# Kernel optimization log

Measured on AMD Instinct MI355X. Metric: run time of the kernel, lower is better.

The kernel has to match this reference:

```python
import jax, jax.numpy as jnp
import numpy as np

N = 50000
E = 800000
IN_C, HID, OUT_C = 512, 256, 128


def gcn_conv(x, edge_index, W, b, num_nodes):
    # PyG GCNConv: add self-loops, symmetric normalization, linear-then-aggregate.
    h = x @ W  # [N, out]
    src = jnp.concatenate([edge_index[0], jnp.arange(num_nodes)])
    dst = jnp.concatenate([edge_index[1], jnp.arange(num_nodes)])
    ones = jnp.ones(src.shape[0], dtype=x.dtype)
    deg = jax.ops.segment_sum(ones, dst, num_segments=num_nodes)  # in-degree incl. self-loop
    dinv = jax.lax.rsqrt(deg)  # deg >= 1 thanks to self-loops
    norm = dinv[src] * dinv[dst]  # [E+N]
    msg = h[src] * norm[:, None]  # gather + scale
    out = jax.ops.segment_sum(msg, dst, num_segments=num_nodes)  # scatter-add
    return out + b


def setup_inputs() -> dict:
    key = jax.random.key(0)
    k_x, k_e, k_w1, k_b1, k_w2, k_b2 = jax.random.split(key, 6)
    x = jax.random.normal(k_x, (N, IN_C), dtype=jnp.float32)
    edge_index = jax.random.randint(k_e, (2, E), 0, N, dtype=jnp.int64)
    s1 = 1.0 / np.sqrt(IN_C)
    s2 = 1.0 / np.sqrt(HID)
    W1 = jax.random.uniform(k_w1, (IN_C, HID), jnp.float32, -s1, s1)
    b1 = jax.random.uniform(k_b1, (HID,), jnp.float32, -s1, s1)
    W2 = jax.random.uniform(k_w2, (HID, OUT_C), jnp.float32, -s2, s2)
    b2 = jax.random.uniform(k_b2, (OUT_C,), jnp.float32, -s2, s2)
    return {"x": x, "edge_index": edge_index, "W1": W1, "b1": b1, "W2": W2, "b2": b2}


def reference(x, edge_index, W1, b1, W2, b2):
    h = gcn_conv(x, edge_index, W1, b1, N)
    h = jax.nn.relu(h)
    # dropout in eval mode == identity
    return gcn_conv(h, edge_index, W2, b2, N)
```

## Files before the change

kernel.cpp:

```cpp
#include <hip/hip_runtime.h>
#include <stdint.h>

typedef __bf16 bf16_t;
typedef bf16_t bf16x8 __attribute__((ext_vector_type(8)));
typedef bf16_t bf16x4 __attribute__((ext_vector_type(4)));
typedef bf16_t bf16x2 __attribute__((ext_vector_type(2)));
typedef float  f32x4  __attribute__((ext_vector_type(4)));

typedef __attribute__((address_space(3))) void* as3p;
typedef const __attribute__((address_space(1))) void* as1p;

#define IN_C 512
#define HID  256
#define OUTC 128

__global__ void k_prep(const float* __restrict__ W1, const float* __restrict__ W2,
                       const void* __restrict__ ei, int* __restrict__ flag,
                       int* __restrict__ cnt, bf16_t* __restrict__ W1t,
                       bf16_t* __restrict__ W2t, int n) {
  int t = blockIdx.x * blockDim.x + threadIdx.x;
  if (t < IN_C * HID) {
    W1t[(size_t)(t & 255) * IN_C + (t >> 8)] = (bf16_t)W1[t];
    return;
  }
  int u = t - IN_C * HID;
  if (u < HID * OUTC) {
    W2t[(size_t)(u & 127) * HID + (u >> 7)] = (bf16_t)W2[u];
    return;
  }
  u -= HID * OUTC;
  if (u < n) {
    cnt[u] = 0;
    return;
  }
  if (u == n) {
    const long long* p = (const long long*)ei;
    int ok = 1;
    for (int i = 0; i < 64; ++i) {
      long long v = p[i];
      if (v < 0 || v >= n) ok = 0;
    }
    *flag = ok;
  }
}

__global__ void k_hist(const void* __restrict__ ei, const int* __restrict__ flag,
                       int* __restrict__ cnt, int E) {
  int e = blockIdx.x * blockDim.x + threadIdx.x;
  if (e >= E) return;
  int d;
  if (*flag) d = (int)((const long long*)ei)[(size_t)E + e];
  else       d = ((const int*)ei)[E + e];
  atomicAdd(&cnt[d], 1);
}

__global__ void k_scan1(const int* __restrict__ cnt, int* __restrict__ ex,
                        int* __restrict__ part, float* __restrict__ dinv, int n) {
  __shared__ int sh[256];
  int i = blockIdx.x * 256 + threadIdx.x;
  int v = (i < n) ? cnt[i] : 0;
  if (i < n) dinv[i] = rsqrtf((float)v + 1.0f);
  sh[threadIdx.x] = v;
  __syncthreads();
  int val = v;
  for (int off = 1; off < 256; off <<= 1) {
    int t = (threadIdx.x >= off) ? sh[threadIdx.x - off] : 0;
    __syncthreads();
    val += t;
    sh[threadIdx.x] = val;
    __syncthreads();
  }
  if (i < n) ex[i] = val - v;
  if (threadIdx.x == 255) part[blockIdx.x] = val;
}

__global__ void k_scan23(int* __restrict__ rs, const int* __restrict__ part,
                         int* __restrict__ cur, int n, int Etot) {
  __shared__ int sh[256];
  const int b = blockIdx.x, t = threadIdx.x;
  int p = 0;
  for (int j = t; j < b; j += 256) p += part[j];
  sh[t] = p;
  __syncthreads();
  for (int off = 128; off > 0; off >>= 1) {
    if (t < off) sh[t] += sh[t + off];
    __syncthreads();
  }
  int base = sh[0];
  int i = b * 256 + t;
  if (i < n) {
    int r = rs[i] + base;
    rs[i] = r;
    cur[i] = r;
  }
  if (i == 0) rs[n] = Etot;
}

__global__ void k_fill(const void* __restrict__ ei, const int* __restrict__ flag,
                       int* __restrict__ cur, int2* __restrict__ csrw,
                       const float* __restrict__ dinv, int E) {
  int e = blockIdx.x * blockDim.x + threadIdx.x;
  if (e >= E) return;
  int s, d;
  if (*flag) {
    const long long* p = (const long long*)ei;
    s = (int)p[e];
    d = (int)p[(size_t)E + e];
  } else {
    const int* p = (const int*)ei;
    s = p[e];
    d = p[E + e];
  }
  int pos = atomicAdd(&cur[d], 1);
  int2 v;
  v.x = s;
  v.y = __float_as_int(dinv[s]);
  csrw[pos] = v;
}

__global__ __launch_bounds__(512, 2) void k_gemm1(const float* __restrict__ A,
                                                  const bf16_t* __restrict__ Bt,
                                                  bf16_t* __restrict__ C, int n) {
  __shared__ float  As[128 * 32];
  __shared__ bf16_t Bs[256 * 32];
  const int bm = blockIdx.x;
  const int tid = threadIdx.x;
  const int wave = tid >> 6, lane = tid & 63;
  const int wm = (wave >> 2) * 64, wn = (wave & 3) * 64;
  const int quad = lane >> 4, l16 = lane & 15;
  const int rowclamp = n - 1;

  f32x4 acc[4][4];
#pragma unroll
  for (int i = 0; i < 4; ++i)
#pragma unroll
    for (int j = 0; j < 4; ++j)
#pragma unroll
      for (int r = 0; r < 4; ++r) acc[i][j][r] = 0.0f;

  for (int kk = 0; kk < IN_C; kk += 32) {
#pragma unroll
    for (int i = 0; i < 2; ++i) {
      int g = i * 512 + tid;
      int rat = g >> 3, ca = g & 7;
      int garow = bm * 128 + rat;
      if (garow > rowclamp) garow = rowclamp;
      const float* srcA = A + (size_t)garow * IN_C + kk + ((ca ^ (rat & 7)) << 2);
      __builtin_amdgcn_global_load_lds((as1p)srcA,
                                       (as3p)(As + (size_t)(i * 512 + wave * 64) * 4), 16, 0, 0);
      int rbt = g >> 2, cb = g & 3;
      const bf16_t* srcB = Bt + (size_t)rbt * IN_C + kk + ((cb ^ ((rbt >> 1) & 3)) << 3);
      __builtin_amdgcn_global_load_lds((as1p)srcB,
                                       (as3p)(Bs + (size_t)(i * 512 + wave * 64) * 8), 16, 0, 0);
    }
    __syncthreads();
    bf16x8 af[4], bfr[4];
#pragma unroll
    for (int i = 0; i < 4; ++i) {
      int ra = wm + i * 16 + l16;
      const float* base = As + ra * 32;
      int s = ra & 7;
      f32x4 v0 = *(const f32x4*)(base + (((quad * 2) ^ s) << 2));
      f32x4 v1 = *(const f32x4*)(base + (((quad * 2 + 1) ^ s) << 2));
      bf16x8 a;
      a[0] = (bf16_t)v0[0]; a[1] = (bf16_t)v0[1]; a[2] = (bf16_t)v0[2]; a[3] = (bf16_t)v0[3];
      a[4] = (bf16_t)v1[0]; a[5] = (bf16_t)v1[1]; a[6] = (bf16_t)v1[2]; a[7] = (bf16_t)v1[3];
      af[i] = a;
    }
#pragma unroll
    for (int j = 0; j < 4; ++j) {
      int rb = wn + j * 16 + l16;
      bfr[j] = *(const bf16x8*)(Bs + rb * 32 + ((quad ^ ((rb >> 1) & 3)) << 3));
    }
#pragma unroll
    for (int i = 0; i < 4; ++i)
#pragma unroll
      for (int j = 0; j < 4; ++j)
        acc[i][j] = __builtin_amdgcn_mfma_f32_16x16x32_bf16(af[i], bfr[j], acc[i][j], 0, 0, 0);
    __syncthreads();
  }

#pragma unroll
  for (int i = 0; i < 4; ++i) {
#pragma unroll
    for (int j = 0; j < 4; ++j) {
      int col = wn + j * 16 + l16;
      int row0 = bm * 128 + wm + i * 16 + quad * 4;
#pragma unroll
      for (int r = 0; r < 4; ++r)
        C[(size_t)(row0 + r) * HID + col] = (bf16_t)acc[i][j][r];
    }
  }
}

__global__ __launch_bounds__(256, 3) void k_gemm(const bf16_t* __restrict__ A,
                                                 const bf16_t* __restrict__ Bt,
                                                 bf16_t* __restrict__ C,
                                                 int Kdim, int Ncols) {
  __shared__ bf16_t As[128 * 32];
  __shared__ bf16_t Bs[128 * 32];
  const int bm = blockIdx.x, bn = blockIdx.y;
  const int tid = threadIdx.x;
  const int wave = tid >> 6, lane = tid & 63;
  const int wm = (wave >> 1) * 64, wn = (wave & 1) * 64;
  const int quad = lane >> 4, l16 = lane & 15;

  const size_t abase = (size_t)bm * 128 * Kdim;
  const size_t bbase = (size_t)bn * 128 * Kdim;

  f32x4 acc[4][4];
#pragma unroll
  for (int i = 0; i < 4; ++i)
#pragma unroll
    for (int j = 0; j < 4; ++j)
#pragma unroll
      for (int r = 0; r < 4; ++r) acc[i][j][r] = 0.0f;

  for (int kk = 0; kk < Kdim; kk += 32) {
#pragma unroll
    for (int i = 0; i < 2; ++i) {
      int g = i * 256 + tid;
      int row = g >> 2, col = (g & 3) * 8;
      const bf16_t* ga = A + abase + (size_t)row * Kdim + kk + col;
      __builtin_amdgcn_global_load_lds((as1p)ga,
                                       (as3p)(&As[(i * 256 + wave * 64) * 8]), 16, 0, 0);
      const bf16_t* gb = Bt + bbase + (size_t)row * Kdim + kk + col;
      __builtin_amdgcn_global_load_lds((as1p)gb,
                                       (as3p)(&Bs[(i * 256 + wave * 64) * 8]), 16, 0, 0);
    }
    __syncthreads();
    bf16x8 af[4], bf[4];
#pragma unroll
    for (int i = 0; i < 4; ++i)
      af[i] = *(const bf16x8*)(&As[(wm + i * 16 + l16) * 32 + quad * 8]);
#pragma unroll
    for (int j = 0; j < 4; ++j)
      bf[j] = *(const bf16x8*)(&Bs[(wn + j * 16 + l16) * 32 + quad * 8]);
#pragma unroll
    for (int i = 0; i < 4; ++i)
#pragma unroll
      for (int j = 0; j < 4; ++j)
        acc[i][j] = __builtin_amdgcn_mfma_f32_16x16x32_bf16(af[i], bf[j], acc[i][j], 0, 0, 0);
    __syncthreads();
  }

#pragma unroll
  for (int i = 0; i < 4; ++i) {
#pragma unroll
    for (int j = 0; j < 4; ++j) {
      int col = bn * 128 + wn + j * 16 + l16;
      int row0 = bm * 128 + wm + i * 16 + quad * 4;
#pragma unroll
      for (int r = 0; r < 4; ++r)
        C[(size_t)(row0 + r) * Ncols + col] = (bf16_t)acc[i][j][r];
    }
  }
}

__global__ void k_agg_l1(const bf16_t* __restrict__ H, const int* __restrict__ rs,
                         const int2* __restrict__ csrw, const float* __restrict__ dinv,
                         const float* __restrict__ b1, bf16_t* __restrict__ R,
                         int n, int mpad, int c0) {
  int d = blockIdx.x * 4 + (threadIdx.x >> 6);
  if (d >= mpad) return;
  const int lane = threadIdx.x & 63;
  const int q = (lane >> 4) & 3;
  const int fl = lane & 15;
  const bf16_t* Hc = H + c0;
  if (d >= n) {
    if (lane < 16) {
      bf16x8 z;
#pragma unroll
      for (int j = 0; j < 8; ++j) z[j] = (bf16_t)0.0f;
      *(bf16x8*)(R + (size_t)d * HID + c0 + fl * 8) = z;
    }
    return;
  }
  int e0 = rs[d], e1 = rs[d + 1];
  float acc0[8], acc1[8];
#pragma unroll
  for (int j = 0; j < 8; ++j) { acc0[j] = 0.f; acc1[j] = 0.f; }
  for (int e = e0; e < e1; e += 32) {
    int2 cw[8];
    float w[8];
    bf16x8 h[8];
#pragma unroll
    for (int u = 0; u < 8; ++u) {
      int idx = e + 4 * u + q;
      int ce = idx < e1 ? idx : e1 - 1;
      cw[u] = csrw[ce];
      w[u] = idx < e1 ? __int_as_float(cw[u].y) : 0.0f;
    }
#pragma unroll
    for (int u = 0; u < 8; ++u)
      h[u] = *(const bf16x8*)(Hc + (size_t)cw[u].x * HID + fl * 8);
#pragma unroll
    for (int u = 0; u < 8; ++u) {
      float* A = (u & 1) ? acc1 : acc0;
#pragma unroll
      for (int j = 0; j < 8; ++j) A[j] += w[u] * (float)h[u][j];
    }
  }
  float a[8];
#pragma unroll
  for (int j = 0; j < 8; ++j) a[j] = acc0[j] + acc1[j];
#pragma unroll
  for (int j = 0; j < 8; ++j) a[j] += __shfl_xor(a[j], 16);
#pragma unroll
  for (int j = 0; j < 8; ++j) a[j] += __shfl_xor(a[j], 32);
  float dd = dinv[d];
  float dv2 = dd * dd;
  bf16x8 hs = *(const bf16x8*)(Hc + (size_t)d * HID + fl * 8);
  float4 bb0 = ((const float4*)(b1 + c0))[fl * 2];
  float4 bb1 = ((const float4*)(b1 + c0))[fl * 2 + 1];
  float bbv[8] = {bb0.x, bb0.y, bb0.z, bb0.w, bb1.x, bb1.y, bb1.z, bb1.w};
  bf16x8 o;
#pragma unroll
  for (int j = 0; j < 8; ++j)
    o[j] = (bf16_t)fmaxf(a[j] * dd + dv2 * (float)hs[j] + bbv[j], 0.f);
  if (lane < 16)
    *(bf16x8*)(R + (size_t)d * HID + c0 + fl * 8) = o;
}

__global__ void k_agg_l2(const bf16_t* __restrict__ H, const int* __restrict__ rs,
                         const int2* __restrict__ csrw, const float* __restrict__ dinv,
                         const float* __restrict__ b2, float* __restrict__ out, int n) {
  int d = blockIdx.x * 4 + (threadIdx.x >> 6);
  if (d >= n) return;
  const int lane = threadIdx.x & 63;
  const int q = (lane >> 4) & 3;
  const int fl = lane & 15;
  int e0 = rs[d], e1 = rs[d + 1];
  float acc0[8], acc1[8];
#pragma unroll
  for (int j = 0; j < 8; ++j) { acc0[j] = 0.f; acc1[j] = 0.f; }
  for (int e = e0; e < e1; e += 32) {
    int2 cw[8];
    float w[8];
    bf16x8 h[8];
#pragma unroll
    for (int u = 0; u < 8; ++u) {
      int idx = e + 4 * u + q;
      int ce = idx < e1 ? idx : e1 - 1;
      cw[u] = csrw[ce];
      w[u] = idx < e1 ? __int_as_float(cw[u].y) : 0.0f;
    }
#pragma unroll
    for (int u = 0; u < 8; ++u)
      h[u] = *(const bf16x8*)(H + (size_t)cw[u].x * OUTC + fl * 8);
#pragma unroll
    for (int u = 0; u < 8; ++u) {
      float* A = (u & 1) ? acc1 : acc0;
#pragma unroll
      for (int j = 0; j < 8; ++j) A[j] += w[u] * (float)h[u][j];
    }
  }
  float a[8];
#pragma unroll
  for (int j = 0; j < 8; ++j) a[j] = acc0[j] + acc1[j];
#pragma unroll
  for (int j = 0; j < 8; ++j) a[j] += __shfl_xor(a[j], 16);
#pragma unroll
  for (int j = 0; j < 8; ++j) a[j] += __shfl_xor(a[j], 32);
  float dd = dinv[d];
  float dv2 = dd * dd;
  bf16x8 hs = *(const bf16x8*)(H + (size_t)d * OUTC + fl * 8);
  float4 bb0 = ((const float4*)b2)[fl * 2];
  float4 bb1 = ((const float4*)b2)[fl * 2 + 1];
  float bbv[8] = {bb0.x, bb0.y, bb0.z, bb0.w, bb1.x, bb1.y, bb1.z, bb1.w};
  float4 o0, o1;
  o0.x = a[0] * dd + dv2 * (float)hs[0] + bbv[0];
  o0.y = a[1] * dd + dv2 * (float)hs[1] + bbv[1];
  o0.z = a[2] * dd + dv2 * (float)hs[2] + bbv[2];
  o0.w = a[3] * dd + dv2 * (float)hs[3] + bbv[3];
  o1.x = a[4] * dd + dv2 * (float)hs[4] + bbv[4];
  o1.y = a[5] * dd + dv2 * (float)hs[5] + bbv[5];
  o1.z = a[6] * dd + dv2 * (float)hs[6] + bbv[6];
  o1.w = a[7] * dd + dv2 * (float)hs[7] + bbv[7];
  if (lane < 16) {
    ((float4*)(out + (size_t)d * OUTC))[fl * 2] = o0;
    ((float4*)(out + (size_t)d * OUTC))[fl * 2 + 1] = o1;
  }
}

extern "C" void kernel_launch(void* const* d_in, const int* in_sizes, int n_in,
                              void* d_out, int out_size, void* d_ws, size_t ws_size,
                              hipStream_t stream) {
  const float* x  = (const float*)d_in[0];
  const void*  ei = d_in[1];
  const float* W1 = (const float*)d_in[2];
  const float* b1 = (const float*)d_in[3];
  const float* W2 = (const float*)d_in[4];
  const float* b2 = (const float*)d_in[5];

  const int n = in_sizes[0] / IN_C;
  const int E = in_sizes[1] / 2;
  const int mpad = (n + 127) & ~127;

  char* w = (char*)d_ws;
  size_t off = 0;
  auto alloc = [&](size_t bytes) -> void* {
    void* p = w + off;
    off = (off + bytes + 255) & ~(size_t)255;
    return p;
  };

  int*    flag = (int*)alloc(4);
  int*    cnt  = (int*)alloc((size_t)n * 4);
  float*  dinv = (float*)alloc((size_t)n * 4);
  int*    rs   = (int*)alloc((size_t)(n + 1) * 4);
  int*    cur  = (int*)alloc((size_t)n * 4);
  int*    part = (int*)alloc(1024);
  int2*   csrw = (int2*)alloc((size_t)E * 8);
  bf16_t* W1t  = (bf16_t*)alloc((size_t)HID * IN_C * 2);
  bf16_t* W2t  = (bf16_t*)alloc((size_t)OUTC * HID * 2);
  bf16_t* H1b  = (bf16_t*)alloc((size_t)mpad * HID * 2);
  bf16_t* R1b  = (bf16_t*)alloc((size_t)mpad * HID * 2);
  bf16_t* H2b  = (bf16_t*)alloc((size_t)mpad * OUTC * 2);
  (void)ws_size; (void)n_in; (void)out_size;

  const int nb = (n + 255) / 256;
  const int prepT = IN_C * HID + HID * OUTC + n + 1;

  k_prep<<<(prepT + 255) / 256, 256, 0, stream>>>(W1, W2, ei, flag, cnt, W1t, W2t, n);
  k_hist<<<(E + 255) / 256, 256, 0, stream>>>(ei, flag, cnt, E);
  k_scan1<<<nb, 256, 0, stream>>>(cnt, rs, part, dinv, n);
  k_scan23<<<nb, 256, 0, stream>>>(rs, part, cur, n, E);
  k_fill<<<(E + 255) / 256, 256, 0, stream>>>(ei, flag, cur, csrw, dinv, E);

  k_gemm1<<<mpad / 128, 512, 0, stream>>>(x, W1t, H1b, n);
  k_agg_l1<<<(mpad + 3) / 4, 256, 0, stream>>>(H1b, rs, csrw, dinv, b1, R1b, n, mpad, 0);
  k_agg_l1<<<(mpad + 3) / 4, 256, 0, stream>>>(H1b, rs, csrw, dinv, b1, R1b, n, mpad, 128);
  k_gemm<<<dim3(mpad / 128, 1), 256, 0, stream>>>(R1b, W2t, H2b, HID, OUTC);
  k_agg_l2<<<(n + 3) / 4, 256, 0, stream>>>(H2b, rs, csrw, dinv, b2, (float*)d_out, n);
}
```

Measured before the change: 385.5 us.

## Split aggregation into narrow column slices with multi-node waves

Rewrites both aggregation kernels so that each block handles a 32-column slice for 32 destination nodes, and each wave loops over 8 nodes. Slice index is interleaved in blockIdx, and layer 1 becomes a single launch instead of two. The intent is better cache locality of gathered feature rows across concurrently running slices. In exchange, each lane does narrow 4-byte gathers, and the CSR index reads are repeated once per slice.

```diff
diff --git a/kernel.cpp b/kernel.cpp
--- a/kernel.cpp
+++ b/kernel.cpp
@@ -260,126 +260,112 @@
 __global__ void k_agg_l1(const bf16_t* __restrict__ H, const int* __restrict__ rs,
                          const int2* __restrict__ csrw, const float* __restrict__ dinv,
                          const float* __restrict__ b1, bf16_t* __restrict__ R,
-                         int n, int mpad, int c0) {
-  int d = blockIdx.x * 4 + (threadIdx.x >> 6);
-  if (d >= mpad) return;
+                         int n, int mpad) {
+  const int slice = blockIdx.x & 7;
+  const int group = blockIdx.x >> 3;
+  const int wave = threadIdx.x >> 6;
   const int lane = threadIdx.x & 63;
   const int q = (lane >> 4) & 3;
   const int fl = lane & 15;
-  const bf16_t* Hc = H + c0;
-  if (d >= n) {
-    if (lane < 16) {
-      bf16x8 z;
-#pragma unroll
-      for (int j = 0; j < 8; ++j) z[j] = (bf16_t)0.0f;
-      *(bf16x8*)(R + (size_t)d * HID + c0 + fl * 8) = z;
-    }
-    return;
-  }
-  int e0 = rs[d], e1 = rs[d + 1];
-  float acc0[8], acc1[8];
-#pragma unroll
-  for (int j = 0; j < 8; ++j) { acc0[j] = 0.f; acc1[j] = 0.f; }
-  for (int e = e0; e < e1; e += 32) {
-    int2 cw[8];
-    float w[8];
-    bf16x8 h[8];
-#pragma unroll
-    for (int u = 0; u < 8; ++u) {
-      int idx = e + 4 * u + q;
-      int ce = idx < e1 ? idx : e1 - 1;
-      cw[u] = csrw[ce];
-      w[u] = idx < e1 ? __int_as_float(cw[u].y) : 0.0f;
-    }
-#pragma unroll
-    for (int u = 0; u < 8; ++u)
-      h[u] = *(const bf16x8*)(Hc + (size_t)cw[u].x * HID + fl * 8);
-#pragma unroll
-    for (int u = 0; u < 8; ++u) {
-      float* A = (u & 1) ? acc1 : acc0;
-#pragma unroll
-      for (int j = 0; j < 8; ++j) A[j] += w[u] * (float)h[u][j];
-    }
-  }
-  float a[8];
-#pragma unroll
-  for (int j = 0; j < 8; ++j) a[j] = acc0[j] + acc1[j];
-#pragma unroll
-  for (int j = 0; j < 8; ++j) a[j] += __shfl_xor(a[j], 16);
-#pragma unroll
-  for (int j = 0; j < 8; ++j) a[j] += __shfl_xor(a[j], 32);
-  float dd = dinv[d];
-  float dv2 = dd * dd;
-  bf16x8 hs = *(const bf16x8*)(Hc + (size_t)d * HID + fl * 8);
-  float4 bb0 = ((const float4*)(b1 + c0))[fl * 2];
-  float4 bb1 = ((const float4*)(b1 + c0))[fl * 2 + 1];
-  float bbv[8] = {bb0.x, bb0.y, bb0.z, bb0.w, bb1.x, bb1.y, bb1.z, bb1.w};
-  bf16x8 o;
-#pragma unroll
-  for (int j = 0; j < 8; ++j)
-    o[j] = (bf16_t)fmaxf(a[j] * dd + dv2 * (float)hs[j] + bbv[j], 0.f);
-  if (lane < 16)
-    *(bf16x8*)(R + (size_t)d * HID + c0 + fl * 8) = o;
+  const int c0 = slice * 32;
+  const bf16_t* Hc = H + c0 + fl * 2;
+  for (int i = 0; i < 8; ++i) {
+    int d = group * 32 + wave * 8 + i;
+    if (d >= mpad) return;
+    if (d >= n) {
+      if (q == 0) {
+        bf16x2 z;
+        z[0] = (bf16_t)0.0f; z[1] = (bf16_t)0.0f;
+        *(bf16x2*)(R + (size_t)d * HID + c0 + fl * 2) = z;
+      }
+      continue;
+    }
+    int e0 = rs[d], e1 = rs[d + 1];
+    float p0 = 0.f, p1 = 0.f, r0 = 0.f, r1 = 0.f;
+    for (int e = e0; e < e1; e += 32) {
+      int2 cw[8];
+      float w[8];
+      bf16x2 h[8];
+#pragma unroll
+      for (int u = 0; u < 8; ++u) {
+        int idx = e + 4 * u + q;
+        int ce = idx < e1 ? idx : e1 - 1;
+        cw[u] = csrw[ce];
+        w[u] = idx < e1 ? __int_as_float(cw[u].y) : 0.0f;
+      }
+#pragma unroll
+      for (int u = 0; u < 8; ++u)
+        h[u] = *(const bf16x2*)(Hc + (size_t)cw[u].x * HID);
+#pragma unroll
+      for (int u = 0; u < 8; ++u) {
+        if (u & 1) { r0 += w[u] * (float)h[u][0]; r1 += w[u] * (float)h[u][1]; }
+        else       { p0 += w[u] * (float)h[u][0]; p1 += w[u] * (float)h[u][1]; }
+      }
+    }
+    float f0 = p0 + r0, f1 = p1 + r1;
+    f0 += __shfl_xor(f0, 16); f1 += __shfl_xor(f1, 16);
+    f0 += __shfl_xor(f0, 32); f1 += __shfl_xor(f1, 32);
+    float dd = dinv[d];
+    float dv2 = dd * dd;
+    bf16x2 hs = *(const bf16x2*)(Hc + (size_t)d * HID);
+    float2 bb = ((const float2*)b1)[slice * 16 + fl];
+    float v0 = fmaxf(f0 * dd + dv2 * (float)hs[0] + bb.x, 0.f);
+    float v1 = fmaxf(f1 * dd + dv2 * (float)hs[1] + bb.y, 0.f);
+    bf16x2 o;
+    o[0] = (bf16_t)v0; o[1] = (bf16_t)v1;
+    if (q == 0)
+      *(bf16x2*)(R + (size_t)d * HID + c0 + fl * 2) = o;
+  }
 }
 
 __global__ void k_agg_l2(const bf16_t* __restrict__ H, const int* __restrict__ rs,
                          const int2* __restrict__ csrw, const float* __restrict__ dinv,
                          const float* __restrict__ b2, float* __restrict__ out, int n) {
-  int d = blockIdx.x * 4 + (threadIdx.x >> 6);
-  if (d >= n) return;
+  const int slice = blockIdx.x & 3;
+  const int group = blockIdx.x >> 2;
+  const int wave = threadIdx.x >> 6;
   const int lane = threadIdx.x & 63;
   const int q = (lane >> 4) & 3;
   const int fl = lane & 15;
-  int e0 = rs[d], e1 = rs[d + 1];
-  float acc0[8], acc1[8];
-#pragma unroll
-  for (int j = 0; j < 8; ++j) { acc0[j] = 0.f; acc1[j] = 0.f; }
-  for (int e = e0; e < e1; e += 32) {
-    int2 cw[8];
-    float w[8];
-    bf16x8 h[8];
-#pragma unroll
-    for (int u = 0; u < 8; ++u) {
-      int idx = e + 4 * u + q;
-      int ce = idx < e1 ? idx : e1 - 1;
-      cw[u] = csrw[ce];
-      w[u] = idx < e1 ? __int_as_float(cw[u].y) : 0.0f;
-    }
-#pragma unroll
-    for (int u = 0; u < 8; ++u)
-      h[u] = *(const bf16x8*)(H + (size_t)cw[u].x * OUTC + fl * 8);
-#pragma unroll
-    for (int u = 0; u < 8; ++u) {
-      float* A = (u & 1) ? acc1 : acc0;
-#pragma unroll
-      for (int j = 0; j < 8; ++j) A[j] += w[u] * (float)h[u][j];
-    }
-  }
-  float a[8];
-#pragma unroll
-  for (int j = 0; j < 8; ++j) a[j] = acc0[j] + acc1[j];
-#pragma unroll
-  for (int j = 0; j < 8; ++j) a[j] += __shfl_xor(a[j], 16);
-#pragma unroll
-  for (int j = 0; j < 8; ++j) a[j] += __shfl_xor(a[j], 32);
-  float dd = dinv[d];
-  float dv2 = dd * dd;
-  bf16x8 hs = *(const bf16x8*)(H + (size_t)d * OUTC + fl * 8);
-  float4 bb0 = ((const float4*)b2)[fl * 2];
-  float4 bb1 = ((const float4*)b2)[fl * 2 + 1];
-  float bbv[8] = {bb0.x, bb0.y, bb0.z, bb0.w, bb1.x, bb1.y, bb1.z, bb1.w};
-  float4 o0, o1;
-  o0.x = a[0] * dd + dv2 * (float)hs[0] + bbv[0];
-  o0.y = a[1] * dd + dv2 * (float)hs[1] + bbv[1];
-  o0.z = a[2] * dd + dv2 * (float)hs[2] + bbv[2];
-  o0.w = a[3] * dd + dv2 * (float)hs[3] + bbv[3];
-  o1.x = a[4] * dd + dv2 * (float)hs[4] + bbv[4];
-  o1.y = a[5] * dd + dv2 * (float)hs[5] + bbv[5];
-  o1.z = a[6] * dd + dv2 * (float)hs[6] + bbv[6];
-  o1.w = a[7] * dd + dv2 * (float)hs[7] + bbv[7];
-  if (lane < 16) {
-    ((float4*)(out + (size_t)d * OUTC))[fl * 2] = o0;
-    ((float4*)(out + (size_t)d * OUTC))[fl * 2 + 1] = o1;
+  const int c0 = slice * 32;
+  const bf16_t* Hc = H + c0 + fl * 2;
+  for (int i = 0; i < 8; ++i) {
+    int d = group * 32 + wave * 8 + i;
+    if (d >= n) return;
+    int e0 = rs[d], e1 = rs[d + 1];
+    float p0 = 0.f, p1 = 0.f, r0 = 0.f, r1 = 0.f;
+    for (int e = e0; e < e1; e += 32) {
+      int2 cw[8];
+      float w[8];
+      bf16x2 h[8];
+#pragma unroll
+      for (int u = 0; u < 8; ++u) {
+        int idx = e + 4 * u + q;
+        int ce = idx < e1 ? idx : e1 - 1;
+        cw[u] = csrw[ce];
+        w[u] = idx < e1 ? __int_as_float(cw[u].y) : 0.0f;
+      }
+#pragma unroll
+      for (int u = 0; u < 8; ++u)
+        h[u] = *(const bf16x2*)(Hc + (size_t)cw[u].x * OUTC);
+#pragma unroll
+      for (int u = 0; u < 8; ++u) {
+        if (u & 1) { r0 += w[u] * (float)h[u][0]; r1 += w[u] * (float)h[u][1]; }
+        else       { p0 += w[u] * (float)h[u][0]; p1 += w[u] * (float)h[u][1]; }
+      }
+    }
+    float f0 = p0 + r0, f1 = p1 + r1;
+    f0 += __shfl_xor(f0, 16); f1 += __shfl_xor(f1, 16);
+    f0 += __shfl_xor(f0, 32); f1 += __shfl_xor(f1, 32);
+    float dd = dinv[d];
+    float dv2 = dd * dd;
+    bf16x2 hs = *(const bf16x2*)(Hc + (size_t)d * OUTC);
+    float2 bb = ((const float2*)b2)[slice * 16 + fl];
+    float2 o;
+    o.x = f0 * dd + dv2 * (float)hs[0] + bb.x;
+    o.y = f1 * dd + dv2 * (float)hs[1] + bb.y;
+    if (q == 0)
+      ((float2*)(out + (size_t)d * OUTC + c0))[fl] = o;
   }
 }
 
@@ -429,8 +415,7 @@
   k_fill<<<(E + 255) / 256, 256, 0, stream>>>(ei, flag, cur, csrw, dinv, E);
 
   k_gemm1<<<mpad / 128, 512, 0, stream>>>(x, W1t, H1b, n);
-  k_agg_l1<<<(mpad + 3) / 4, 256, 0, stream>>>(H1b, rs, csrw, dinv, b1, R1b, n, mpad, 0);
-  k_agg_l1<<<(mpad + 3) / 4, 256, 0, stream>>>(H1b, rs, csrw, dinv, b1, R1b, n, mpad, 128);
+  k_agg_l1<<<8 * ((mpad + 31) / 32), 256, 0, stream>>>(H1b, rs, csrw, dinv, b1, R1b, n, mpad);
   k_gemm<<<dim3(mpad / 128, 1), 256, 0, stream>>>(R1b, W2t, H2b, HID, OUTC);
-  k_agg_l2<<<(n + 3) / 4, 256, 0, stream>>>(H2b, rs, csrw, dinv, b2, (float*)d_out, n);
-}
+  k_agg_l2<<<4 * ((n + 31) / 32), 256, 0, stream>>>(H2b, rs, csrw, dinv, b2, (float*)d_out, n);
+}
```

New measurement: 453.2 us. 17.6% more time.
